# Performance work log

Measured on AMD Instinct MI355X. Metric: run time of the kernel, lower is better.

Reference implementation:

```python
import jax, jax.numpy as jnp
import numpy as np

NUM_HEADS = 12
EPS = 1e-6


def _rms_norm(x, w):
    # RMSNorm over the full channel dim (applied before head split), fp32 math
    return x * jax.lax.rsqrt(jnp.mean(x * x, axis=-1, keepdims=True) + EPS) * w


def _rope_apply(t, F, H, W, freqs):
    # t: [B, S, n, d] with S == F*H*W; freqs: [1024, d//2] angles
    B, S, n, d = t.shape
    c = d // 2
    s0 = c - 2 * (c // 3)  # temporal split (22 when d=128)
    s1 = c // 3            # spatial splits (21, 21)
    f0, f1, f2 = freqs[:, :s0], freqs[:, s0:s0 + s1], freqs[:, s0 + s1:]
    ang = jnp.concatenate([
        jnp.broadcast_to(f0[:F, None, None, :], (F, H, W, s0)),
        jnp.broadcast_to(f1[None, :H, None, :], (F, H, W, s1)),
        jnp.broadcast_to(f2[None, None, :W, :], (F, H, W, s1)),
    ], axis=-1).reshape(S, c)                      # [S, c]
    cos = jnp.cos(ang)[None, :, None, :]           # [1, S, 1, c]
    sin = jnp.sin(ang)[None, :, None, :]
    tp = t.reshape(B, S, n, c, 2)
    te, to = tp[..., 0], tp[..., 1]                # complex (real, imag) pairs
    rot = jnp.stack([te * cos - to * sin, te * sin + to * cos], axis=-1)
    return rot.reshape(B, S, n, d)


def reference(x, seq_lens, grid_sizes, freqs, Wq, bq, Wk, bk, Wv, bv, Wo, bo, norm_q_w, norm_k_w):
    B, S, C = x.shape
    n = NUM_HEADS
    d = C // n
    gs = np.asarray(grid_sizes)[0]
    F, H, W = int(gs[0]), int(gs[1]), int(gs[2])  # static: L == F*H*W, same per sample

    q = _rms_norm(x @ Wq.T + bq, norm_q_w).reshape(B, S, n, d)
    k = _rms_norm(x @ Wk.T + bk, norm_k_w).reshape(B, S, n, d)
    v = (x @ Wv.T + bv).reshape(B, S, n, d)

    q = _rope_apply(q, F, H, W, freqs)
    k = _rope_apply(k, F, H, W, freqs)

    scale = 1.0 / jnp.sqrt(jnp.float32(d))
    scores = jnp.einsum('bqnd,bknd->bnqk', q, k) * scale   # [B, n, S, S]
    kmask = jnp.arange(S)[None, :] < seq_lens[:, None]      # [B, S] valid keys
    scores = jnp.where(kmask[:, None, None, :], scores, -jnp.inf)
    attn = jax.nn.softmax(scores, axis=-1)
    out = jnp.einsum('bnqk,bknd->bqnd', attn, v).reshape(B, S, C)
    return out @ Wo.T + bo


def setup_inputs() -> dict:
    key = jax.random.key(0)
    ks = jax.random.split(key, 10)
    B, F, H, W = 2, 4, 24, 32
    S = F * H * W  # 3072
    C = 1536
    d = C // NUM_HEADS  # 128
    c = d // 2          # 64

    x = jax.random.normal(ks[0], (B, S, C), dtype=jnp.float32)
    seq_lens = jnp.array([S, 2500], dtype=jnp.int32)
    grid_sizes = jnp.array([[F, H, W]] * B, dtype=jnp.int32)

    # rope angles: outer(pos, 1/theta^(2i/dim)) per split [22, 21, 21]
    def rope_params(max_len, dim_k, theta=10000.0):
        inv = 1.0 / (theta ** (np.arange(0, dim_k, 2, dtype=np.float64) / dim_k))
        return np.outer(np.arange(max_len), inv)
    s0 = c - 2 * (c // 3)
    s1 = c // 3
    freqs = jnp.asarray(np.concatenate([
        rope_params(1024, 2 * s0), rope_params(1024, 2 * s1), rope_params(1024, 2 * s1)
    ], axis=1), dtype=jnp.float32)  # [1024, 64]

    std = 0.02
    def lin(k):
        return jax.random.normal(k, (C, C), dtype=jnp.float32) * std
    return {
        'x': x, 'seq_lens': seq_lens, 'grid_sizes': grid_sizes, 'freqs': freqs,
        'Wq': lin(ks[1]), 'bq': jnp.zeros((C,), jnp.float32),
        'Wk': lin(ks[2]), 'bk': jnp.zeros((C,), jnp.float32),
        'Wv': lin(ks[3]), 'bv': jnp.zeros((C,), jnp.float32),
        'Wo': lin(ks[4]), 'bo': jnp.zeros((C,), jnp.float32),
        'norm_q_w': jnp.ones((C,), jnp.float32),
        'norm_k_w': jnp.ones((C,), jnp.float32),
    }
```

## Files before the change

### kernel.cpp

```cpp
#include <hip/hip_runtime.h>
#include <hip/hip_bf16.h>
#include <math.h>

#define NB 2
#define SS 3072
#define CC 1536
#define NH 12
#define DH 128
#define NTOK (NB * SS)
#define WE (CC * CC)
#define LOG2E 1.4426950408889634f
#define QBLK 192

typedef __attribute__((ext_vector_type(8))) short short8;
typedef __attribute__((ext_vector_type(4))) float floatx4;

#define GLOAD(g, l) __builtin_amdgcn_global_load_lds( \
    (const __attribute__((address_space(1))) void*)(g), \
    (__attribute__((address_space(3))) void*)(l), 16, 0, 0)

__device__ __forceinline__ unsigned short f2bf(float f) {
    unsigned u = __float_as_uint(f);
    u += 0x7fffu + ((u >> 16) & 1u);
    return (unsigned short)(u >> 16);
}
__device__ __forceinline__ int swz(int row, int q) {
    return row * 4 + (q ^ ((row >> 1) & 3));
}

__global__ __launch_bounds__(256) void cast_all(
    const float* __restrict__ x,
    const float* __restrict__ w0, const float* __restrict__ w1,
    const float* __restrict__ w2, const float* __restrict__ w3,
    unsigned short* __restrict__ o)
{
    const int y = blockIdx.y;
    const float* src = (y < 4) ? x + (size_t)y * WE
                     : (y == 4) ? w0 : (y == 5) ? w1 : (y == 6) ? w2 : w3;
    size_t i = ((size_t)blockIdx.x * 256 + threadIdx.x) * 4;
    float4 v = *(const float4*)&src[i];
    uint2 u;
    u.x = (unsigned)f2bf(v.x) | ((unsigned)f2bf(v.y) << 16);
    u.y = (unsigned)f2bf(v.z) | ((unsigned)f2bf(v.w) << 16);
    *(uint2*)&o[(size_t)y * WE + i] = u;
}

__global__ __launch_bounds__(256) void rope_table(
    const float* __restrict__ freqs, const int* __restrict__ gsz,
    float2* __restrict__ tab)
{
    const int id = blockIdx.x * 256 + threadIdx.x;
    const int s = id >> 6, pj = id & 63;
    const int Hg = gsz[1], Wg = gsz[2];
    const int f = s / (Hg * Wg);
    const int rem = s - f * Hg * Wg;
    const int hh = rem / Wg;
    const int ww = rem - hh * Wg;
    const int row = (pj < 22) ? f : ((pj < 43) ? hh : ww);
    float sn, cs;
    sincosf(freqs[row * 64 + pj], &sn, &cs);
    tab[id] = make_float2(cs, sn);
}

__global__ __launch_bounds__(256) void qkv_gemm(
    const unsigned short* __restrict__ X,
    const unsigned short* __restrict__ Wqb, const unsigned short* __restrict__ Wkb,
    const unsigned short* __restrict__ Wvb,
    const float* __restrict__ bq, const float* __restrict__ bk,
    const float* __restrict__ bv,
    unsigned short* __restrict__ qo, unsigned short* __restrict__ ko,
    unsigned short* __restrict__ vto)
{
    __shared__ unsigned short As[128 * 32];
    __shared__ unsigned short Bs[128 * 32];
    const int tid = threadIdx.x;
    const int w = tid >> 6, l = tid & 63;
    const int jseg = blockIdx.y / 12;
    const unsigned short* Wt = (jseg == 0) ? Wqb : (jseg == 1) ? Wkb : Wvb;
    const float* bias        = (jseg == 0) ? bq  : (jseg == 1) ? bk  : bv;
    unsigned short* Y        = (jseg == 0) ? qo  : (jseg == 1) ? ko  : vto;
    const int i0 = blockIdx.x * 128, j0 = (blockIdx.y % 12) * 128;
    const int srow = tid >> 2;
    const int gk8 = (((tid & 3) ^ ((srow >> 1) & 3))) * 8;

    floatx4 acc[4][4] = {};
    for (int k0 = 0; k0 < CC; k0 += 32) {
        __syncthreads();
        GLOAD(X + (size_t)(i0 + srow) * CC + k0 + gk8,        As + (size_t)tid * 8);
        GLOAD(X + (size_t)(i0 + 64 + srow) * CC + k0 + gk8,   As + (size_t)(256 + tid) * 8);
        GLOAD(Wt + (size_t)(j0 + srow) * CC + k0 + gk8,       Bs + (size_t)tid * 8);
        GLOAD(Wt + (size_t)(j0 + 64 + srow) * CC + k0 + gk8,  Bs + (size_t)(256 + tid) * 8);
        __syncthreads();
        const int wr = (w >> 1) * 64, wc = (w & 1) * 64;
        short8 af[4], bf[4];
        #pragma unroll
        for (int mb = 0; mb < 4; ++mb)
            af[mb] = *(const short8*)&As[swz(wr + mb * 16 + (l & 15), l >> 4) * 8];
        #pragma unroll
        for (int nb = 0; nb < 4; ++nb)
            bf[nb] = *(const short8*)&Bs[swz(wc + nb * 16 + (l & 15), l >> 4) * 8];
        #pragma unroll
        for (int mb = 0; mb < 4; ++mb)
            #pragma unroll
            for (int nb = 0; nb < 4; ++nb)
                acc[mb][nb] = __builtin_amdgcn_mfma_f32_16x16x32_bf16(
                    af[mb], bf[nb], acc[mb][nb], 0, 0, 0);
    }

    const int wr = (w >> 1) * 64, wc = (w & 1) * 64;
    #pragma unroll
    for (int mb = 0; mb < 4; ++mb)
        #pragma unroll
        for (int nb = 0; nb < 4; ++nb) {
            const int n = j0 + wc + nb * 16 + (l & 15);
            const float bv2 = bias[n];
            const int h = n >> 7, td = n & 127;
            #pragma unroll
            for (int r = 0; r < 4; ++r) {
                const int m = i0 + wr + mb * 16 + (l >> 4) * 4 + r;
                const float val = acc[mb][nb][r] + bv2;
                const int b = (m >= SS) ? 1 : 0;
                const int s = m - b * SS;
                if (jseg < 2)
                    Y[((size_t)(b * NH + h) * SS + s) * DH + td] = f2bf(val);
                else
                    Y[((size_t)(b * NH + h) * DH + td) * SS + s] = f2bf(val);
            }
        }
}

__global__ __launch_bounds__(256) void gemm_o(
    const unsigned short* __restrict__ X, const unsigned short* __restrict__ Wt,
    const float* __restrict__ bias, float* __restrict__ Y)
{
    __shared__ unsigned short As[128 * 32];
    __shared__ unsigned short Bs[128 * 32];
    const int tid = threadIdx.x;
    const int w = tid >> 6, l = tid & 63;
    const int i0 = blockIdx.x * 128, j0 = blockIdx.y * 128;
    const int srow = tid >> 2;
    const int gk8 = (((tid & 3) ^ ((srow >> 1) & 3))) * 8;

    floatx4 acc[4][4] = {};
    for (int k0 = 0; k0 < CC; k0 += 32) {
        __syncthreads();
        GLOAD(X + (size_t)(i0 + srow) * CC + k0 + gk8,        As + (size_t)tid * 8);
        GLOAD(X + (size_t)(i0 + 64 + srow) * CC + k0 + gk8,   As + (size_t)(256 + tid) * 8);
        GLOAD(Wt + (size_t)(j0 + srow) * CC + k0 + gk8,       Bs + (size_t)tid * 8);
        GLOAD(Wt + (size_t)(j0 + 64 + srow) * CC + k0 + gk8,  Bs + (size_t)(256 + tid) * 8);
        __syncthreads();
        const int wr = (w >> 1) * 64, wc = (w & 1) * 64;
        short8 af[4], bf[4];
        #pragma unroll
        for (int mb = 0; mb < 4; ++mb)
            af[mb] = *(const short8*)&As[swz(wr + mb * 16 + (l & 15), l >> 4) * 8];
        #pragma unroll
        for (int nb = 0; nb < 4; ++nb)
            bf[nb] = *(const short8*)&Bs[swz(wc + nb * 16 + (l & 15), l >> 4) * 8];
        #pragma unroll
        for (int mb = 0; mb < 4; ++mb)
            #pragma unroll
            for (int nb = 0; nb < 4; ++nb)
                acc[mb][nb] = __builtin_amdgcn_mfma_f32_16x16x32_bf16(
                    af[mb], bf[nb], acc[mb][nb], 0, 0, 0);
    }

    const int wr = (w >> 1) * 64, wc = (w & 1) * 64;
    #pragma unroll
    for (int mb = 0; mb < 4; ++mb)
        #pragma unroll
        for (int nb = 0; nb < 4; ++nb) {
            const int n = j0 + wc + nb * 16 + (l & 15);
            const float bv = bias[n];
            #pragma unroll
            for (int r = 0; r < 4; ++r) {
                const int m = i0 + wr + mb * 16 + (l >> 4) * 4 + r;
                Y[(size_t)m * CC + n] = acc[mb][nb][r] + bv;
            }
        }
}

__global__ __launch_bounds__(256) void norm_rope(
    unsigned short* __restrict__ qb, unsigned short* __restrict__ kb,
    const float* __restrict__ nqw, const float* __restrict__ nkw,
    const float2* __restrict__ tab)
{
    const int bid = blockIdx.x;
    const int which = (bid >= NTOK) ? 1 : 0;
    const int tok = bid - which * NTOK;
    unsigned short* t    = which ? kb : qb;
    const float* wgt     = which ? nkw : nqw;
    const float outscale = which ? 1.0f : 0.08838834764831845f * LOG2E;
    const int b = tok / SS, s = tok - b * SS;
    const int tid = threadIdx.x;

    float2 vals[3];
    size_t addrs[3];
    float ss = 0.f;
    #pragma unroll
    for (int kt = 0; kt < 3; ++kt) {
        int p = tid + kt * 256;
        int h = p >> 6, pj = p & 63;
        size_t addr = ((size_t)(b * NH + h) * SS + s) * DH + 2 * pj;
        addrs[kt] = addr;
        unsigned u = *(const unsigned*)&t[addr];
        float2 v;
        v.x = __uint_as_float(u << 16);
        v.y = __uint_as_float(u & 0xffff0000u);
        vals[kt] = v;
        ss += v.x * v.x + v.y * v.y;
    }
    #pragma unroll
    for (int off = 32; off > 0; off >>= 1) ss += __shfl_down(ss, off, 64);
    __shared__ float red[4];
    if ((tid & 63) == 0) red[tid >> 6] = ss;
    __syncthreads();
    const float total = red[0] + red[1] + red[2] + red[3];
    const float rstd = rsqrtf(total * (1.0f / CC) + 1e-6f) * outscale;

    #pragma unroll
    for (int kt = 0; kt < 3; ++kt) {
        int p = tid + kt * 256;
        int h = p >> 6, pj = p & 63;
        float2 cssn = tab[s * 64 + pj];
        int ch = h * DH + 2 * pj;
        float te = vals[kt].x * rstd * wgt[ch];
        float to = vals[kt].y * rstd * wgt[ch + 1];
        unsigned o = (unsigned)f2bf(te * cssn.x - to * cssn.y) |
                     ((unsigned)f2bf(te * cssn.y + to * cssn.x) << 16);
        *(unsigned*)&t[addrs[kt]] = o;
    }
}

__global__ __launch_bounds__(256, 2) void flash_attn_mfma(
    const unsigned short* __restrict__ qg, const unsigned short* __restrict__ kg,
    const unsigned short* __restrict__ vg, const int* __restrict__ seq_lens,
    unsigned short* __restrict__ out)
{
    __shared__ unsigned short lds[32768];
    const int tid = threadIdx.x;
    const int w = tid >> 6, l = tid & 63;
    const int g4 = (l >> 4) * 4;

    const int bid = blockIdx.x;
    const int qt = bid / (NB * NH);
    const int rem0 = bid - qt * (NB * NH);
    const int h = rem0 >> 1;
    const int b = rem0 & 1;
    const int slen = seq_lens[b];
    const int s0 = qt * QBLK;

    const unsigned short* qbase = qg + ((size_t)(b * NH + h) * SS + s0) * DH;
    const unsigned short* kbase = kg + ((size_t)(b * NH + h) * SS) * DH;
    const unsigned short* vbase = vg + ((size_t)(b * NH + h) * DH) * SS;

    #pragma unroll
    for (int i = 0; i < 12; ++i) {
        int kc = i / 3;
        int r2 = (i % 3) * 256 + tid;
        int row = r2 >> 2, sq = r2 & 3;
        GLOAD(qbase + (size_t)row * DH + kc * 32 + (sq ^ ((row >> 1) & 3)) * 8,
              lds + (size_t)(kc * 768 + r2) * 8);
    }
    __syncthreads();
    short8 qf[3][4];
    #pragma unroll
    for (int rb = 0; rb < 3; ++rb)
        #pragma unroll
        for (int kc = 0; kc < 4; ++kc)
            qf[rb][kc] = *(const short8*)&lds[(kc * 768 + swz(w * 48 + rb * 16 + (l & 15), l >> 4)) * 8];
    __syncthreads();

    int ksrc[4], vsrc[4];
    #pragma unroll
    for (int i = 0; i < 4; ++i) {
        int cid = i * 256 + tid;
        {   int kc = cid >> 8, r2 = cid & 255, row = r2 >> 2, sq = r2 & 3;
            ksrc[i] = row * DH + kc * 32 + (sq ^ ((row >> 1) & 3)) * 8; }
        {   int ks = cid >> 9, r2 = cid & 511, dc = r2 >> 2, sq = r2 & 3;
            vsrc[i] = dc * SS + ks * 32 + (sq ^ ((dc >> 1) & 3)) * 8; }
    }

    const int ntiles = (slen + 63) >> 6;

    #pragma unroll
    for (int i = 0; i < 4; ++i) {
        int cid = i * 256 + tid;
        GLOAD(kbase + ksrc[i],        lds + (size_t)cid * 8);
        GLOAD(vbase + vsrc[i],        lds + 8192 + (size_t)cid * 8);
    }

    floatx4 acc[3][8] = {};
    float lsum[3] = {};

    for (int kt = 0; kt < ntiles; ++kt) {
        __syncthreads();

        if (kt + 1 < ntiles) {
            const unsigned short* kb2 = kbase + (size_t)(kt + 1) * 64 * DH;
            const unsigned short* vb2 = vbase + (size_t)(kt + 1) * 64;
            unsigned short* dst = lds + ((kt + 1) & 1) * 16384;
            #pragma unroll
            for (int i = 0; i < 4; ++i) {
                int cid = i * 256 + tid;
                GLOAD(kb2 + ksrc[i], dst + (size_t)cid * 8);
                GLOAD(vb2 + vsrc[i], dst + 8192 + (size_t)cid * 8);
            }
        }

        const unsigned short* Ks = lds + (kt & 1) * 16384;
        const unsigned short* Vs = Ks + 8192;

        floatx4 sv[3][4] = {};
        __builtin_amdgcn_s_setprio(1);
        #pragma unroll
        for (int kc = 0; kc < 4; ++kc) {
            short8 kf[4];
            #pragma unroll
            for (int nb = 0; nb < 4; ++nb)
                kf[nb] = *(const short8*)&Ks[(kc * 256 + swz(nb * 16 + (l & 15), l >> 4)) * 8];
            #pragma unroll
            for (int rb = 0; rb < 3; ++rb)
                #pragma unroll
                for (int nb = 0; nb < 4; ++nb)
                    sv[rb][nb] = __builtin_amdgcn_mfma_f32_16x16x32_bf16(
                        kf[nb], qf[rb][kc], sv[rb][nb], 0, 0, 0);
        }
        __builtin_amdgcn_s_setprio(0);

        const int valid = slen - kt * 64;
        short8 pa[3][2];
        #pragma unroll
        for (int rb = 0; rb < 3; ++rb) {
            if (valid >= 64) {
                #pragma unroll
                for (int nb = 0; nb < 4; ++nb)
                    #pragma unroll
                    for (int r = 0; r < 4; ++r)
                        sv[rb][nb][r] = exp2f(sv[rb][nb][r]);
            } else {
                #pragma unroll
                for (int nb = 0; nb < 4; ++nb)
                    #pragma unroll
                    for (int r = 0; r < 4; ++r) {
                        const int key = g4 + r + 16 * nb;
                        sv[rb][nb][r] = (key < valid) ? exp2f(sv[rb][nb][r]) : 0.0f;
                    }
            }
            #pragma unroll
            for (int nb = 0; nb < 4; ++nb)
                lsum[rb] += (sv[rb][nb][0] + sv[rb][nb][1]) +
                            (sv[rb][nb][2] + sv[rb][nb][3]);

            unsigned dw0[4], dw1[4];
            #pragma unroll
            for (int nb = 0; nb < 4; ++nb) {
                union { __hip_bfloat162 v; unsigned u; } c0, c1;
                c0.v = __float22bfloat162_rn(make_float2(sv[rb][nb][0], sv[rb][nb][1]));
                c1.v = __float22bfloat162_rn(make_float2(sv[rb][nb][2], sv[rb][nb][3]));
                dw0[nb] = c0.u;
                dw1[nb] = c1.u;
            }
            #pragma unroll
            for (int ks = 0; ks < 2; ++ks) {
                unsigned x0 = dw0[2 * ks], y0 = dw0[2 * ks + 1];
                unsigned x1 = dw1[2 * ks], y1 = dw1[2 * ks + 1];
                asm("v_permlane32_swap_b32 %0, %1" : "+v"(x0), "+v"(y0));
                asm("v_permlane16_swap_b32 %0, %1" : "+v"(x0), "+v"(y0));
                asm("v_permlane32_swap_b32 %0, %1" : "+v"(x1), "+v"(y1));
                asm("v_permlane16_swap_b32 %0, %1" : "+v"(x1), "+v"(y1));
                union { short8 s; unsigned u[4]; } pk;
                pk.u[0] = x0; pk.u[1] = x1; pk.u[2] = y0; pk.u[3] = y1;
                pa[rb][ks] = pk.s;
            }
        }

        __builtin_amdgcn_s_setprio(1);
        #pragma unroll
        for (int ks = 0; ks < 2; ++ks)
            #pragma unroll
            for (int nb2 = 0; nb2 < 8; ++nb2) {
                short8 vf = *(const short8*)&Vs[(ks * 512 + swz(nb2 * 16 + (l & 15), l >> 4)) * 8];
                #pragma unroll
                for (int rb = 0; rb < 3; ++rb)
                    acc[rb][nb2] = __builtin_amdgcn_mfma_f32_16x16x32_bf16(
                        pa[rb][ks], vf, acc[rb][nb2], 0, 0, 0);
            }
        __builtin_amdgcn_s_setprio(0);
    }

    #pragma unroll
    for (int rb = 0; rb < 3; ++rb) {
        float s = lsum[rb];
        s += __shfl_xor(s, 16, 64);
        s += __shfl_xor(s, 32, 64);
        float rl[4];
        #pragma unroll
        for (int r = 0; r < 4; ++r)
            rl[r] = 1.0f / __shfl(s, g4 + r, 64);
        #pragma unroll
        for (int nb2 = 0; nb2 < 8; ++nb2) {
            const int col = h * DH + nb2 * 16 + (l & 15);
            #pragma unroll
            for (int r = 0; r < 4; ++r) {
                const int srow = s0 + w * 48 + rb * 16 + (l >> 4) * 4 + r;
                out[((size_t)b * SS + srow) * CC + col] = f2bf(acc[rb][nb2][r] * rl[r]);
            }
        }
    }
}

extern "C" void kernel_launch(void* const* d_in, const int* in_sizes, int n_in,
                              void* d_out, int out_size, void* d_ws, size_t ws_size,
                              hipStream_t stream) {
    const float* x          = (const float*)d_in[0];
    const int*   seq_lens   = (const int*)d_in[1];
    const int*   grid_sizes = (const int*)d_in[2];
    const float* freqs      = (const float*)d_in[3];
    const float* Wq         = (const float*)d_in[4];
    const float* bq         = (const float*)d_in[5];
    const float* Wk         = (const float*)d_in[6];
    const float* bk         = (const float*)d_in[7];
    const float* Wv         = (const float*)d_in[8];
    const float* bv         = (const float*)d_in[9];
    const float* Wo         = (const float*)d_in[10];
    const float* bo         = (const float*)d_in[11];
    const float* nqw        = (const float*)d_in[12];
    const float* nkw        = (const float*)d_in[13];
    float* out = (float*)d_out;

    const size_t TE = (size_t)NTOK * CC;
    unsigned short* xb  = (unsigned short*)d_ws;
    unsigned short* wqb = xb + TE;
    unsigned short* wkb = wqb + WE;
    unsigned short* wvb = wkb + WE;
    unsigned short* wob = wvb + WE;
    unsigned short* qb  = wob + WE;
    unsigned short* kb  = qb + TE;
    unsigned short* vtb = kb + TE;
    unsigned short* ab  = vtb + TE;
    float2* tab = (float2*)(ab + TE);

    cast_all<<<dim3(WE / 1024, 8), 256, 0, stream>>>(x, Wq, Wk, Wv, Wo, xb);
    rope_table<<<dim3(SS * 64 / 256), 256, 0, stream>>>(freqs, grid_sizes, tab);

    qkv_gemm<<<dim3(NTOK / 128, 36), 256, 0, stream>>>(
        xb, wqb, wkb, wvb, bq, bk, bv, qb, kb, vtb);

    norm_rope<<<dim3(2 * NTOK), 256, 0, stream>>>(qb, kb, nqw, nkw, tab);

    flash_attn_mfma<<<dim3(NB * NH * (SS / QBLK)), 256, 0, stream>>>(qb, kb, vtb, seq_lens, ab);

    gemm_o<<<dim3(NTOK / 128, CC / 128), 256, 0, stream>>>(ab, wob, bo, out);
}
```

Before: 515.7 us.

## Fuse rope table into cast kernel, merge q/k norm blocks, peel last attention tile

Folds the rope sin/cos table computation into the cast kernel as an extra grid row, which removes one launch. The norm_rope kernel now handles q and k for the same token in one block, halving the block count and sharing table reads. The flash attention loop peels the final key tile so the steady-state loop has no prefetch condition and no masking branch, with pointer-increment prefetch addressing. This adds code size and register pressure in exchange for fewer launches and less control flow.

Result: faster. 487.8 us (-5.4%).

```diff
diff --git a/kernel.cpp b/kernel.cpp
--- a/kernel.cpp
+++ b/kernel.cpp
@@ -28,13 +28,30 @@
     return row * 4 + (q ^ ((row >> 1) & 3));
 }
 
-__global__ __launch_bounds__(256) void cast_all(
+__global__ __launch_bounds__(256) void cast_rope(
     const float* __restrict__ x,
     const float* __restrict__ w0, const float* __restrict__ w1,
     const float* __restrict__ w2, const float* __restrict__ w3,
-    unsigned short* __restrict__ o)
+    unsigned short* __restrict__ o,
+    const float* __restrict__ freqs, const int* __restrict__ gsz,
+    float2* __restrict__ tab)
 {
     const int y = blockIdx.y;
+    if (y == 8) {
+        const int id = blockIdx.x * 256 + threadIdx.x;
+        if (id >= SS * 64) return;
+        const int s = id >> 6, pj = id & 63;
+        const int Hg = gsz[1], Wg = gsz[2];
+        const int f = s / (Hg * Wg);
+        const int rem = s - f * Hg * Wg;
+        const int hh = rem / Wg;
+        const int ww = rem - hh * Wg;
+        const int row = (pj < 22) ? f : ((pj < 43) ? hh : ww);
+        float sn, cs;
+        sincosf(freqs[row * 64 + pj], &sn, &cs);
+        tab[id] = make_float2(cs, sn);
+        return;
+    }
     const float* src = (y < 4) ? x + (size_t)y * WE
                      : (y == 4) ? w0 : (y == 5) ? w1 : (y == 6) ? w2 : w3;
     size_t i = ((size_t)blockIdx.x * 256 + threadIdx.x) * 4;
@@ -43,23 +60,6 @@
     u.x = (unsigned)f2bf(v.x) | ((unsigned)f2bf(v.y) << 16);
     u.y = (unsigned)f2bf(v.z) | ((unsigned)f2bf(v.w) << 16);
     *(uint2*)&o[(size_t)y * WE + i] = u;
-}
-
-__global__ __launch_bounds__(256) void rope_table(
-    const float* __restrict__ freqs, const int* __restrict__ gsz,
-    float2* __restrict__ tab)
-{
-    const int id = blockIdx.x * 256 + threadIdx.x;
-    const int s = id >> 6, pj = id & 63;
-    const int Hg = gsz[1], Wg = gsz[2];
-    const int f = s / (Hg * Wg);
-    const int rem = s - f * Hg * Wg;
-    const int hh = rem / Wg;
-    const int ww = rem - hh * Wg;
-    const int row = (pj < 22) ? f : ((pj < 43) ? hh : ww);
-    float sn, cs;
-    sincosf(freqs[row * 64 + pj], &sn, &cs);
-    tab[id] = make_float2(cs, sn);
 }
 
 __global__ __launch_bounds__(256) void qkv_gemm(
@@ -185,38 +185,41 @@
     const float* __restrict__ nqw, const float* __restrict__ nkw,
     const float2* __restrict__ tab)
 {
-    const int bid = blockIdx.x;
-    const int which = (bid >= NTOK) ? 1 : 0;
-    const int tok = bid - which * NTOK;
-    unsigned short* t    = which ? kb : qb;
-    const float* wgt     = which ? nkw : nqw;
-    const float outscale = which ? 1.0f : 0.08838834764831845f * LOG2E;
+    const int tok = blockIdx.x;
     const int b = tok / SS, s = tok - b * SS;
     const int tid = threadIdx.x;
-
-    float2 vals[3];
+    const float qscale = 0.08838834764831845f * LOG2E;
+
+    float2 qv[3], kv[3];
     size_t addrs[3];
-    float ss = 0.f;
+    float ssq = 0.f, ssk = 0.f;
     #pragma unroll
     for (int kt = 0; kt < 3; ++kt) {
         int p = tid + kt * 256;
         int h = p >> 6, pj = p & 63;
         size_t addr = ((size_t)(b * NH + h) * SS + s) * DH + 2 * pj;
         addrs[kt] = addr;
-        unsigned u = *(const unsigned*)&t[addr];
-        float2 v;
-        v.x = __uint_as_float(u << 16);
-        v.y = __uint_as_float(u & 0xffff0000u);
-        vals[kt] = v;
-        ss += v.x * v.x + v.y * v.y;
-    }
-    #pragma unroll
-    for (int off = 32; off > 0; off >>= 1) ss += __shfl_down(ss, off, 64);
-    __shared__ float red[4];
-    if ((tid & 63) == 0) red[tid >> 6] = ss;
+        unsigned uq = *(const unsigned*)&qb[addr];
+        unsigned uk = *(const unsigned*)&kb[addr];
+        float2 vq, vk;
+        vq.x = __uint_as_float(uq << 16);
+        vq.y = __uint_as_float(uq & 0xffff0000u);
+        vk.x = __uint_as_float(uk << 16);
+        vk.y = __uint_as_float(uk & 0xffff0000u);
+        qv[kt] = vq; kv[kt] = vk;
+        ssq += vq.x * vq.x + vq.y * vq.y;
+        ssk += vk.x * vk.x + vk.y * vk.y;
+    }
+    #pragma unroll
+    for (int off = 32; off > 0; off >>= 1) {
+        ssq += __shfl_down(ssq, off, 64);
+        ssk += __shfl_down(ssk, off, 64);
+    }
+    __shared__ float redq[4], redk[4];
+    if ((tid & 63) == 0) { redq[tid >> 6] = ssq; redk[tid >> 6] = ssk; }
     __syncthreads();
-    const float total = red[0] + red[1] + red[2] + red[3];
-    const float rstd = rsqrtf(total * (1.0f / CC) + 1e-6f) * outscale;
+    const float rq = rsqrtf((redq[0] + redq[1] + redq[2] + redq[3]) * (1.0f / CC) + 1e-6f) * qscale;
+    const float rk = rsqrtf((redk[0] + redk[1] + redk[2] + redk[3]) * (1.0f / CC) + 1e-6f);
 
     #pragma unroll
     for (int kt = 0; kt < 3; ++kt) {
@@ -224,11 +227,20 @@
         int h = p >> 6, pj = p & 63;
         float2 cssn = tab[s * 64 + pj];
         int ch = h * DH + 2 * pj;
-        float te = vals[kt].x * rstd * wgt[ch];
-        float to = vals[kt].y * rstd * wgt[ch + 1];
-        unsigned o = (unsigned)f2bf(te * cssn.x - to * cssn.y) |
-                     ((unsigned)f2bf(te * cssn.y + to * cssn.x) << 16);
-        *(unsigned*)&t[addrs[kt]] = o;
+        {
+            float te = qv[kt].x * rq * nqw[ch];
+            float to = qv[kt].y * rq * nqw[ch + 1];
+            unsigned o = (unsigned)f2bf(te * cssn.x - to * cssn.y) |
+                         ((unsigned)f2bf(te * cssn.y + to * cssn.x) << 16);
+            *(unsigned*)&qb[addrs[kt]] = o;
+        }
+        {
+            float te = kv[kt].x * rk * nkw[ch];
+            float to = kv[kt].y * rk * nkw[ch + 1];
+            unsigned o = (unsigned)f2bf(te * cssn.x - to * cssn.y) |
+                         ((unsigned)f2bf(te * cssn.y + to * cssn.x) << 16);
+            *(unsigned*)&kb[addrs[kt]] = o;
+        }
     }
 }
 
@@ -282,6 +294,7 @@
     }
 
     const int ntiles = (slen + 63) >> 6;
+    const int rem = slen & 63;
 
     #pragma unroll
     for (int i = 0; i < 4; ++i) {
@@ -292,20 +305,22 @@
 
     floatx4 acc[3][8] = {};
     float lsum[3] = {};
-
-    for (int kt = 0; kt < ntiles; ++kt) {
+    const unsigned short* kpf = kbase + (size_t)64 * DH;
+    const unsigned short* vpf = vbase + 64;
+
+    for (int kt = 0; kt < ntiles - 1; ++kt) {
         __syncthreads();
 
-        if (kt + 1 < ntiles) {
-            const unsigned short* kb2 = kbase + (size_t)(kt + 1) * 64 * DH;
-            const unsigned short* vb2 = vbase + (size_t)(kt + 1) * 64;
+        {
             unsigned short* dst = lds + ((kt + 1) & 1) * 16384;
             #pragma unroll
             for (int i = 0; i < 4; ++i) {
                 int cid = i * 256 + tid;
-                GLOAD(kb2 + ksrc[i], dst + (size_t)cid * 8);
-                GLOAD(vb2 + vsrc[i], dst + 8192 + (size_t)cid * 8);
-            }
+                GLOAD(kpf + ksrc[i], dst + (size_t)cid * 8);
+                GLOAD(vpf + vsrc[i], dst + 8192 + (size_t)cid * 8);
+            }
+            kpf += (size_t)64 * DH;
+            vpf += 64;
         }
 
         const unsigned short* Ks = lds + (kt & 1) * 16384;
@@ -328,11 +343,84 @@
         }
         __builtin_amdgcn_s_setprio(0);
 
-        const int valid = slen - kt * 64;
         short8 pa[3][2];
         #pragma unroll
         for (int rb = 0; rb < 3; ++rb) {
-            if (valid >= 64) {
+            #pragma unroll
+            for (int nb = 0; nb < 4; ++nb)
+                #pragma unroll
+                for (int r = 0; r < 4; ++r)
+                    sv[rb][nb][r] = exp2f(sv[rb][nb][r]);
+            #pragma unroll
+            for (int nb = 0; nb < 4; ++nb)
+                lsum[rb] += (sv[rb][nb][0] + sv[rb][nb][1]) +
+                            (sv[rb][nb][2] + sv[rb][nb][3]);
+
+            unsigned dw0[4], dw1[4];
+            #pragma unroll
+            for (int nb = 0; nb < 4; ++nb) {
+                union { __hip_bfloat162 v; unsigned u; } c0, c1;
+                c0.v = __float22bfloat162_rn(make_float2(sv[rb][nb][0], sv[rb][nb][1]));
+                c1.v = __float22bfloat162_rn(make_float2(sv[rb][nb][2], sv[rb][nb][3]));
+                dw0[nb] = c0.u;
+                dw1[nb] = c1.u;
+            }
+            #pragma unroll
+            for (int ks = 0; ks < 2; ++ks) {
+                unsigned x0 = dw0[2 * ks], y0 = dw0[2 * ks + 1];
+                unsigned x1 = dw1[2 * ks], y1 = dw1[2 * ks + 1];
+                asm("v_permlane32_swap_b32 %0, %1" : "+v"(x0), "+v"(y0));
+                asm("v_permlane16_swap_b32 %0, %1" : "+v"(x0), "+v"(y0));
+                asm("v_permlane32_swap_b32 %0, %1" : "+v"(x1), "+v"(y1));
+                asm("v_permlane16_swap_b32 %0, %1" : "+v"(x1), "+v"(y1));
+                union { short8 s; unsigned u[4]; } pk;
+                pk.u[0] = x0; pk.u[1] = x1; pk.u[2] = y0; pk.u[3] = y1;
+                pa[rb][ks] = pk.s;
+            }
+        }
+
+        __builtin_amdgcn_s_setprio(1);
+        #pragma unroll
+        for (int ks = 0; ks < 2; ++ks)
+            #pragma unroll
+            for (int nb2 = 0; nb2 < 8; ++nb2) {
+                short8 vf = *(const short8*)&Vs[(ks * 512 + swz(nb2 * 16 + (l & 15), l >> 4)) * 8];
+                #pragma unroll
+                for (int rb = 0; rb < 3; ++rb)
+                    acc[rb][nb2] = __builtin_amdgcn_mfma_f32_16x16x32_bf16(
+                        pa[rb][ks], vf, acc[rb][nb2], 0, 0, 0);
+            }
+        __builtin_amdgcn_s_setprio(0);
+    }
+
+    {
+        const int kt = ntiles - 1;
+        __syncthreads();
+
+        const unsigned short* Ks = lds + (kt & 1) * 16384;
+        const unsigned short* Vs = Ks + 8192;
+
+        floatx4 sv[3][4] = {};
+        __builtin_amdgcn_s_setprio(1);
+        #pragma unroll
+        for (int kc = 0; kc < 4; ++kc) {
+            short8 kf[4];
+            #pragma unroll
+            for (int nb = 0; nb < 4; ++nb)
+                kf[nb] = *(const short8*)&Ks[(kc * 256 + swz(nb * 16 + (l & 15), l >> 4)) * 8];
+            #pragma unroll
+            for (int rb = 0; rb < 3; ++rb)
+                #pragma unroll
+                for (int nb = 0; nb < 4; ++nb)
+                    sv[rb][nb] = __builtin_amdgcn_mfma_f32_16x16x32_bf16(
+                        kf[nb], qf[rb][kc], sv[rb][nb], 0, 0, 0);
+        }
+        __builtin_amdgcn_s_setprio(0);
+
+        short8 pa[3][2];
+        #pragma unroll
+        for (int rb = 0; rb < 3; ++rb) {
+            if (rem == 0) {
                 #pragma unroll
                 for (int nb = 0; nb < 4; ++nb)
                     #pragma unroll
@@ -344,7 +432,7 @@
                     #pragma unroll
                     for (int r = 0; r < 4; ++r) {
                         const int key = g4 + r + 16 * nb;
-                        sv[rb][nb][r] = (key < valid) ? exp2f(sv[rb][nb][r]) : 0.0f;
+                        sv[rb][nb][r] = (key < rem) ? exp2f(sv[rb][nb][r]) : 0.0f;
                     }
             }
             #pragma unroll
@@ -441,13 +529,13 @@
     unsigned short* ab  = vtb + TE;
     float2* tab = (float2*)(ab + TE);
 
-    cast_all<<<dim3(WE / 1024, 8), 256, 0, stream>>>(x, Wq, Wk, Wv, Wo, xb);
-    rope_table<<<dim3(SS * 64 / 256), 256, 0, stream>>>(freqs, grid_sizes, tab);
+    cast_rope<<<dim3(WE / 1024, 9), 256, 0, stream>>>(
+        x, Wq, Wk, Wv, Wo, xb, freqs, grid_sizes, tab);
 
     qkv_gemm<<<dim3(NTOK / 128, 36), 256, 0, stream>>>(
         xb, wqb, wkb, wvb, bq, bk, bv, qb, kb, vtb);
 
-    norm_rope<<<dim3(2 * NTOK), 256, 0, stream>>>(qb, kb, nqw, nkw, tab);
+    norm_rope<<<dim3(NTOK), 256, 0, stream>>>(qb, kb, nqw, nkw, tab);
 
     flash_attn_mfma<<<dim3(NB * NH * (SS / QBLK)), 256, 0, stream>>>(qb, kb, vtb, seq_lens, ab);
 
```
